# Performance work log

Measured on AMD Instinct MI355X. Metric: run time of the kernel, lower is better.

The kernel has to match this reference:

```python
import jax, jax.numpy as jnp
import numpy as np

EPS = 1e-5

def setup_inputs() -> dict:
    key = jax.random.key(0)
    ks = jax.random.split(key, 6)
    B, S, F, D = 512, 64, 768, 256
    # xavier-ish scales for weights
    return {
        "audio_feat": jax.random.normal(ks[0], (B, S, F), dtype=jnp.float32),
        "visual_feat": jax.random.normal(ks[1], (B, S, F), dtype=jnp.float32),
        "Wa": jax.random.normal(ks[2], (F, D), dtype=jnp.float32) * (1.0 / np.sqrt(F)),
        "ba": jnp.zeros((D,), dtype=jnp.float32),
        "Wv": jax.random.normal(ks[3], (F, D), dtype=jnp.float32) * (1.0 / np.sqrt(F)),
        "bv": jnp.zeros((D,), dtype=jnp.float32),
        "corr": jax.random.normal(ks[4], (D, D), dtype=jnp.float32) * float(np.sqrt(2.0 / (D + D))),
        "Wb": jax.random.normal(ks[5], (2 * D, 64), dtype=jnp.float32) * (1.0 / np.sqrt(2 * D)),
        "bb": jnp.zeros((64,), dtype=jnp.float32),
        "gamma": jnp.ones((64,), dtype=jnp.float32),
        "beta": jnp.zeros((64,), dtype=jnp.float32),
    }


def reference(audio_feat, visual_feat, Wa, ba, Wv, bv, corr, Wb, bb, gamma, beta):
    # project: [b,s,768] -> [b,s,256]
    a = jnp.einsum('bsf,fd->bsd', audio_feat, Wa) + ba      # audio proj
    v = jnp.einsum('bsf,fd->bsd', visual_feat, Wv) + bv     # vision proj
    vT = jnp.swapaxes(v, 1, 2)                              # [b,d,s]
    # bilinear correlation: cc[b,i,j] = a[b,i,:] @ corr @ v[b,j,:]
    cc = jnp.einsum('bid,de,bje->bij', a, corr, v)          # [b,sa,sv]
    audio_att = jax.nn.softmax(cc, axis=1)                  # softmax over audio positions
    visual_att = jax.nn.softmax(cc, axis=2)                 # softmax over visual positions (of cc^T along dim 1)
    # attended features, both [b,d,s]
    att_a = jnp.einsum('bid,bij->bdj', a, audio_att) + jnp.swapaxes(a, 1, 2)
    att_v = jnp.einsum('bdj,bij->bdi', vT, jnp.swapaxes(visual_att, 1, 2))
    # note: bmm(vT [b,d,sv], visual_att^T' ...) -> torch does vT @ visual_att_t where
    # visual_att_t[b,j,i] = visual_att[b,i,j]; equivalent einsum below
    att_v = jnp.einsum('bdj,bji->bdi', vT, jnp.swapaxes(visual_att, 1, 2)) + vT
    fused = jnp.concatenate([att_a, att_v], axis=1)         # [b,2d,s]
    fused = jnp.swapaxes(fused, 1, 2)                       # [b,s,2d]
    h = jnp.einsum('bsk,ko->bso', fused, Wb) + bb           # [b,s,64]
    mu = jnp.mean(h, axis=-1, keepdims=True)
    var = jnp.mean(jnp.square(h - mu), axis=-1, keepdims=True)
    h = (h - mu) * jax.lax.rsqrt(var + EPS) * gamma + beta
    return jax.nn.relu(h)
```

## Files before the change

kernel.cpp:

```cpp
#include <hip/hip_runtime.h>

typedef _Float16 f16x8 __attribute__((ext_vector_type(8)));
typedef _Float16 f16x4 __attribute__((ext_vector_type(4)));
typedef float    f32x4 __attribute__((ext_vector_type(4)));

#define A16_OFF   0u
#define V16_OFF   16777216u
#define WAP_OFF   33554432u
#define WVP_OFF   33947648u
#define CORRT_OFF 34340864u
#define WBT_OFF   34471936u

#define SCHED0() __builtin_amdgcn_sched_barrier(0)
#define SBAR()   __builtin_amdgcn_s_barrier()

__device__ __forceinline__ void gl_lds16(const void* g, void* l) {
    __builtin_amdgcn_global_load_lds(
        (const __attribute__((address_space(1))) void*)g,
        (__attribute__((address_space(3))) void*)l, 16, 0, 0);
}

__global__ __launch_bounds__(256) void k_prep(
    const float* __restrict__ Wa, const float* __restrict__ Wv,
    const float* __restrict__ corr, const float* __restrict__ Wb,
    _Float16* __restrict__ WaP, _Float16* __restrict__ WvP,
    _Float16* __restrict__ corrT, _Float16* __restrict__ WbT)
{
    __shared__ _Float16 tile[64][72];
    int bid = blockIdx.x;
    int t = threadIdx.x;
    if (bid < 192) {
        int z = bid >= 96;
        int b = z ? bid - 96 : bid;
        const float* W = z ? Wv : Wa;
        _Float16* P = z ? WvP : WaP;
        int kc = b >> 2, nbg = b & 3;
        int l = t & 63, sub = t >> 6;
        int nb = nbg * 4 + sub;
        int q = l >> 4, lm = l & 15;
        int k0 = kc * 32 + q * 8;
        int n = nb * 16 + lm;
        _Float16 tmp[8];
        #pragma unroll
        for (int e = 0; e < 8; ++e)
            tmp[e] = (_Float16)W[(size_t)(k0 + e) * 256 + n];
        *reinterpret_cast<f16x8*>(P + ((size_t)(kc * 16 + nb) * 64 + l) * 8) =
            *reinterpret_cast<const f16x8*>(tmp);
    } else {
        int b2 = bid - 192;
        const float* src; _Float16* dst; int R, C, tr, tc;
        if (b2 < 16) { src = corr; dst = corrT; R = 256; C = 256; tr = b2 >> 2; tc = b2 & 3; }
        else         { src = Wb;   dst = WbT;   R = 512; C = 64;  tr = b2 - 16; tc = 0;      }
        int r0 = tr * 64, c0 = tc * 64;
        #pragma unroll
        for (int it = 0; it < 16; ++it) {
            int idx = t + it * 256;
            int r = idx >> 6, c = idx & 63;
            tile[r][c] = (_Float16)src[(size_t)(r0 + r) * C + (c0 + c)];
        }
        __syncthreads();
        #pragma unroll
        for (int it = 0; it < 16; ++it) {
            int idx = t + it * 256;
            int c = idx >> 6, r = idx & 63;
            dst[(size_t)(c0 + c) * R + (r0 + r)] = tile[r][c];
        }
    }
}

__global__ __launch_bounds__(512, 1) void k_proj(
    const float* __restrict__ Xa, const float* __restrict__ Xv,
    const _Float16* __restrict__ WaP, const _Float16* __restrict__ WvP,
    const float* __restrict__ ba, const float* __restrict__ bv,
    _Float16* __restrict__ Aout, _Float16* __restrict__ Vout)
{
    extern __shared__ __align__(16) char smem[];

    const int bid = blockIdx.x;
    const int lin = (bid & 7) * 64 + (bid >> 3);
    const int z = lin >> 8, mb = lin & 255;
    const float*    X    = z ? Xv  : Xa;
    const _Float16* WP   = z ? WvP : WaP;
    const float*    bias = z ? bv  : ba;
    _Float16*       Out  = z ? Vout : Aout;
    const int m0 = mb * 128;

    const int t = threadIdx.x, lane = t & 63, w = t >> 6;
    const int wr = w >> 1, wc = w & 1;
    const int q = lane >> 4, lm = lane & 15;

    f32x4 acc[2][8] = {};

    auto stageA = [&](int ks) {
        char* base = smem + (ks & 3) * 16384;
        #pragma unroll
        for (int it = 0; it < 2; ++it) {
            int idx0 = it * 512 + w * 64;
            int idx = idx0 + lane;
            int r = idx >> 3, c = idx & 7;
            int gc = c ^ (r & 7);
            gl_lds16(X + (size_t)(m0 + r) * 768 + ks * 32 + gc * 4,
                     base + idx0 * 16);
        }
    };
    auto stageB = [&](int ks) {
        char* base = smem + 65536 + (ks & 3) * 16384;
        #pragma unroll
        for (int it = 0; it < 2; ++it) {
            int idx0 = it * 512 + w * 64;
            gl_lds16(WP + ((size_t)ks * 1024 + idx0 + lane) * 8,
                     base + idx0 * 16);
        }
    };

    stageA(0); stageB(0);
    stageA(1); stageB(1);
    stageA(2); stageB(2);
    stageA(3); stageB(3);
    asm volatile("s_waitcnt vmcnt(12)" ::: "memory"); SCHED0();
    SBAR();

    for (int ks = 0; ks < 24; ++ks) {
        const char* Ac = smem + (ks & 3) * 16384;
        const char* Bc = smem + 65536 + (ks & 3) * 16384;

        f16x8 af[2];
        #pragma unroll
        for (int mf = 0; mf < 2; ++mf) {
            int r = wr * 32 + mf * 16 + lm;
            const char* base = Ac + r * 128;
            int c0 = (2 * q) ^ (r & 7);
            int c1 = (2 * q + 1) ^ (r & 7);
            f32x4 lo = *reinterpret_cast<const f32x4*>(base + c0 * 16);
            f32x4 hi = *reinterpret_cast<const f32x4*>(base + c1 * 16);
            f16x4 l4 = __builtin_convertvector(lo, f16x4);
            f16x4 h4 = __builtin_convertvector(hi, f16x4);
            af[mf] = __builtin_shufflevector(l4, h4, 0, 1, 2, 3, 4, 5, 6, 7);
        }
        #pragma unroll
        for (int nf = 0; nf < 8; ++nf) {
            int nb = wc * 8 + nf;
            f16x8 bf = *reinterpret_cast<const f16x8*>(Bc + (nb * 64 + lane) * 16);
            acc[0][nf] = __builtin_amdgcn_mfma_f32_16x16x32_f16(af[0], bf, acc[0][nf], 0, 0, 0);
            acc[1][nf] = __builtin_amdgcn_mfma_f32_16x16x32_f16(af[1], bf, acc[1][nf], 0, 0, 0);
        }
        asm volatile("s_waitcnt lgkmcnt(0)" ::: "memory"); SCHED0();
        SBAR();
        if (ks + 4 < 24) { stageA(ks + 4); stageB(ks + 4); }
        if (ks < 20)      { asm volatile("s_waitcnt vmcnt(12)" ::: "memory"); }
        else if (ks == 20){ asm volatile("s_waitcnt vmcnt(8)"  ::: "memory"); }
        else if (ks == 21){ asm volatile("s_waitcnt vmcnt(4)"  ::: "memory"); }
        else if (ks == 22){ asm volatile("s_waitcnt vmcnt(0)"  ::: "memory"); }
        SCHED0();
        if (ks < 23) SBAR();
    }

    float biasv[8];
    #pragma unroll
    for (int nf = 0; nf < 8; ++nf)
        biasv[nf] = bias[wc * 128 + nf * 16 + lm];

    _Float16* Cs = (_Float16*)smem;
    #pragma unroll
    for (int mf = 0; mf < 2; ++mf)
        #pragma unroll
        for (int nf = 0; nf < 8; ++nf)
            #pragma unroll
            for (int r = 0; r < 4; ++r)
                Cs[(wr * 32 + mf * 16 + q * 4 + r) * 256 + wc * 128 + nf * 16 + lm] =
                    (_Float16)(acc[mf][nf][r] + biasv[nf]);
    __syncthreads();
    #pragma unroll
    for (int it = 0; it < 8; ++it) {
        int idx = t + it * 512;
        int row = idx >> 5, c = idx & 31;
        f16x8 vv = *reinterpret_cast<const f16x8*>(Cs + row * 256 + c * 8);
        *reinterpret_cast<f16x8*>(Out + (size_t)(m0 + row) * 256 + c * 8) = vv;
    }
}

#define SM_A    0u
#define SM_V    33792u
#define SM_AC   67584u
#define SM_CC   101376u
#define SM_ATA  118272u
#define SM_ATV  127488u
#define SM_AWT  136704u
#define SM_VWT  145920u
#define SM_RED  155136u
#define SM_TOTAL 159232u

__global__ __launch_bounds__(256) void k_fuse(
    const _Float16* __restrict__ A16, const _Float16* __restrict__ V16,
    const _Float16* __restrict__ corrT, const _Float16* __restrict__ WbT,
    const float* __restrict__ bb, const float* __restrict__ gamma,
    const float* __restrict__ beta, float* __restrict__ out)
{
    extern __shared__ char sm[];
    _Float16* a_s   = (_Float16*)(sm + SM_A);
    _Float16* v_s   = (_Float16*)(sm + SM_V);
    _Float16* ac_s  = (_Float16*)(sm + SM_AC);
    float*    cc_s  = (float*)(sm + SM_CC);
    _Float16* attAT = (_Float16*)(sm + SM_ATA);
    _Float16* attV  = (_Float16*)(sm + SM_ATV);
    _Float16* awT   = (_Float16*)(sm + SM_AWT);
    _Float16* vwT   = (_Float16*)(sm + SM_VWT);
    float*    red   = (float*)(sm + SM_RED);

    const int b = blockIdx.x;
    const int t = threadIdx.x, lane = t & 63, w = t >> 6;
    const int q = lane >> 4, lm = lane & 15;

    const _Float16* Ab = A16 + (size_t)b * 64 * 256;
    const _Float16* Vb = V16 + (size_t)b * 64 * 256;
    #pragma unroll
    for (int it = 0; it < 8; ++it) {
        int idx = t + it * 256;
        int row = idx >> 5, kc = idx & 31;
        *reinterpret_cast<f16x8*>(a_s + row * 264 + kc * 8) =
            *reinterpret_cast<const f16x8*>(Ab + row * 256 + kc * 8);
        *reinterpret_cast<f16x8*>(v_s + row * 264 + kc * 8) =
            *reinterpret_cast<const f16x8*>(Vb + row * 256 + kc * 8);
    }
    __syncthreads();

    {
        f32x4 acc[4][4] = {};
        for (int ks = 0; ks < 8; ++ks) {
            f16x8 af[4];
            #pragma unroll
            for (int mf = 0; mf < 4; ++mf)
                af[mf] = *reinterpret_cast<const f16x8*>(a_s + (mf * 16 + lm) * 264 + ks * 32 + q * 8);
            #pragma unroll
            for (int nf = 0; nf < 4; ++nf) {
                int e = w * 64 + nf * 16 + lm;
                f16x8 bf = *reinterpret_cast<const f16x8*>(corrT + (size_t)e * 256 + ks * 32 + q * 8);
                #pragma unroll
                for (int mf = 0; mf < 4; ++mf)
                    acc[mf][nf] = __builtin_amdgcn_mfma_f32_16x16x32_f16(af[mf], bf, acc[mf][nf], 0, 0, 0);
            }
        }
        #pragma unroll
        for (int mf = 0; mf < 4; ++mf)
            #pragma unroll
            for (int nf = 0; nf < 4; ++nf)
                #pragma unroll
                for (int r = 0; r < 4; ++r)
                    ac_s[(mf * 16 + 4 * q + r) * 264 + (w * 64 + nf * 16 + lm)] = (_Float16)acc[mf][nf][r];
    }
    __syncthreads();

    {
        f32x4 acc[4] = {};
        for (int ks = 0; ks < 8; ++ks) {
            f16x8 bf = *reinterpret_cast<const f16x8*>(v_s + (w * 16 + lm) * 264 + ks * 32 + q * 8);
            #pragma unroll
            for (int mf = 0; mf < 4; ++mf) {
                f16x8 af = *reinterpret_cast<const f16x8*>(ac_s + (mf * 16 + lm) * 264 + ks * 32 + q * 8);
                acc[mf] = __builtin_amdgcn_mfma_f32_16x16x32_f16(af, bf, acc[mf], 0, 0, 0);
            }
        }
        #pragma unroll
        for (int mf = 0; mf < 4; ++mf)
            #pragma unroll
            for (int r = 0; r < 4; ++r)
                cc_s[(mf * 16 + 4 * q + r) * 66 + (w * 16 + lm)] = acc[mf][r];
    }
    __syncthreads();

    {
        int j = t & 63, seg = w;
        float cmx = -1e30f, rmx = -1e30f;
        #pragma unroll
        for (int k = 0; k < 16; ++k) {
            int i = seg * 16 + k;
            cmx = fmaxf(cmx, cc_s[i * 66 + j]);
            rmx = fmaxf(rmx, cc_s[j * 66 + i]);
        }
        red[0 * 256 + seg * 64 + j] = cmx;
        red[2 * 256 + seg * 64 + j] = rmx;
        __syncthreads();
        float cm = fmaxf(fmaxf(red[0 * 256 + 0 * 64 + j], red[0 * 256 + 1 * 64 + j]),
                         fmaxf(red[0 * 256 + 2 * 64 + j], red[0 * 256 + 3 * 64 + j]));
        float rm = fmaxf(fmaxf(red[2 * 256 + 0 * 64 + j], red[2 * 256 + 1 * 64 + j]),
                         fmaxf(red[2 * 256 + 2 * 64 + j], red[2 * 256 + 3 * 64 + j]));
        float cs = 0.f, rs = 0.f;
        #pragma unroll
        for (int k = 0; k < 16; ++k) {
            int i = seg * 16 + k;
            cs += __expf(cc_s[i * 66 + j] - cm);
            rs += __expf(cc_s[j * 66 + i] - rm);
        }
        red[1 * 256 + seg * 64 + j] = cs;
        red[3 * 256 + seg * 64 + j] = rs;
        __syncthreads();
        float csum = red[1 * 256 + 0 * 64 + j] + red[1 * 256 + 1 * 64 + j] +
                     red[1 * 256 + 2 * 64 + j] + red[1 * 256 + 3 * 64 + j];
        float rsum = red[3 * 256 + 0 * 64 + j] + red[3 * 256 + 1 * 64 + j] +
                     red[3 * 256 + 2 * 64 + j] + red[3 * 256 + 3 * 64 + j];
        float cinv = 1.f / csum, rinv = 1.f / rsum;
        #pragma unroll
        for (int k = 0; k < 16; ++k) {
            int i = seg * 16 + k;
            float pa = __expf(cc_s[i * 66 + j] - cm) * cinv;
            if (i == j) pa += 1.f;
            attAT[j * 72 + i] = (_Float16)pa;
            float pv = __expf(cc_s[j * 66 + i] - rm) * rinv;
            if (i == j) pv += 1.f;
            attV[j * 72 + i] = (_Float16)pv;
        }
    }

    {
        int isV = w >> 1, wcol = w & 1;
        const _Float16* src = isV ? v_s : a_s;
        const int doff = isV ? 256 : 0;
        f32x4 acc[4][2] = {};
        for (int ks = 0; ks < 8; ++ks) {
            f16x8 af[4];
            #pragma unroll
            for (int mf = 0; mf < 4; ++mf)
                af[mf] = *reinterpret_cast<const f16x8*>(src + (mf * 16 + lm) * 264 + ks * 32 + q * 8);
            #pragma unroll
            for (int nf = 0; nf < 2; ++nf) {
                int o = wcol * 32 + nf * 16 + lm;
                f16x8 bf = *reinterpret_cast<const f16x8*>(WbT + (size_t)o * 512 + doff + ks * 32 + q * 8);
                #pragma unroll
                for (int mf = 0; mf < 4; ++mf)
                    acc[mf][nf] = __builtin_amdgcn_mfma_f32_16x16x32_f16(af[mf], bf, acc[mf][nf], 0, 0, 0);
            }
        }
        _Float16* dst = isV ? vwT : awT;
        #pragma unroll
        for (int mf = 0; mf < 4; ++mf)
            #pragma unroll
            for (int nf = 0; nf < 2; ++nf)
                #pragma unroll
                for (int r = 0; r < 4; ++r)
                    dst[(wcol * 32 + nf * 16 + lm) * 72 + (mf * 16 + 4 * q + r)] = (_Float16)acc[mf][nf][r];
    }
    __syncthreads();

    f32x4 hacc[4] = {};
    #pragma unroll
    for (int kk = 0; kk < 2; ++kk) {
        f16x8 a1 = *reinterpret_cast<const f16x8*>(attAT + (16 * w + lm) * 72 + kk * 32 + q * 8);
        f16x8 a2 = *reinterpret_cast<const f16x8*>(attV  + (16 * w + lm) * 72 + kk * 32 + q * 8);
        #pragma unroll
        for (int nf = 0; nf < 4; ++nf) {
            f16x8 b1 = *reinterpret_cast<const f16x8*>(awT + (nf * 16 + lm) * 72 + kk * 32 + q * 8);
            f16x8 b2 = *reinterpret_cast<const f16x8*>(vwT + (nf * 16 + lm) * 72 + kk * 32 + q * 8);
            hacc[nf] = __builtin_amdgcn_mfma_f32_16x16x32_f16(a1, b1, hacc[nf], 0, 0, 0);
            hacc[nf] = __builtin_amdgcn_mfma_f32_16x16x32_f16(a2, b2, hacc[nf], 0, 0, 0);
        }
    }

    {
        float bbv[4], gv[4], bev[4];
        #pragma unroll
        for (int nf = 0; nf < 4; ++nf) {
            int o = nf * 16 + lm;
            bbv[nf] = bb[o]; gv[nf] = gamma[o]; bev[nf] = beta[o];
        }
        #pragma unroll
        for (int r = 0; r < 4; ++r) {
            float vals[4]; float s1 = 0.f, s2 = 0.f;
            #pragma unroll
            for (int nf = 0; nf < 4; ++nf) {
                float hv = hacc[nf][r] + bbv[nf];
                vals[nf] = hv; s1 += hv; s2 += hv * hv;
            }
            #pragma unroll
            for (int m = 1; m < 16; m <<= 1) {
                s1 += __shfl_xor(s1, m, 64);
                s2 += __shfl_xor(s2, m, 64);
            }
            float mu = s1 * 0.015625f;
            float var = s2 * 0.015625f - mu * mu;
            float rstd = rsqrtf(var + 1e-5f);
            int s = 16 * w + 4 * q + r;
            float* orow = out + ((size_t)b * 64 + s) * 64;
            #pragma unroll
            for (int nf = 0; nf < 4; ++nf) {
                float y = (vals[nf] - mu) * rstd * gv[nf] + bev[nf];
                orow[nf * 16 + lm] = fmaxf(y, 0.f);
            }
        }
    }
}

extern "C" void kernel_launch(void* const* d_in, const int* in_sizes, int n_in,
                              void* d_out, int out_size, void* d_ws, size_t ws_size,
                              hipStream_t stream) {
    const float* Xa    = (const float*)d_in[0];
    const float* Xv    = (const float*)d_in[1];
    const float* Wa    = (const float*)d_in[2];
    const float* ba    = (const float*)d_in[3];
    const float* Wv    = (const float*)d_in[4];
    const float* bv    = (const float*)d_in[5];
    const float* corr  = (const float*)d_in[6];
    const float* Wb    = (const float*)d_in[7];
    const float* bb    = (const float*)d_in[8];
    const float* gamma = (const float*)d_in[9];
    const float* beta  = (const float*)d_in[10];
    float* out = (float*)d_out;
    char* ws = (char*)d_ws;

    _Float16* a16   = (_Float16*)(ws + A16_OFF);
    _Float16* v16   = (_Float16*)(ws + V16_OFF);
    _Float16* WaP   = (_Float16*)(ws + WAP_OFF);
    _Float16* WvP   = (_Float16*)(ws + WVP_OFF);
    _Float16* corrT = (_Float16*)(ws + CORRT_OFF);
    _Float16* WbT   = (_Float16*)(ws + WBT_OFF);

    hipLaunchKernelGGL(k_prep, dim3(216), dim3(256), 0, stream,
                       Wa, Wv, corr, Wb, WaP, WvP, corrT, WbT);
    (void)hipFuncSetAttribute((const void*)k_proj,
                              hipFuncAttributeMaxDynamicSharedMemorySize, 131072);
    hipLaunchKernelGGL(k_proj, dim3(512), dim3(512), 131072, stream,
                       Xa, Xv, WaP, WvP, ba, bv, a16, v16);
    (void)hipFuncSetAttribute((const void*)k_fuse,
                              hipFuncAttributeMaxDynamicSharedMemorySize, SM_TOTAL);
    hipLaunchKernelGGL(k_fuse, dim3(512), dim3(256), SM_TOTAL, stream,
                       a16, v16, corrT, WbT, bb, gamma, beta, out);
}
```

Baseline: 92.74 us.

## Restructure projection GEMM pipeline with register-staged A loads and K=64 steps

The projection GEMM's main loop now advances 64 K-elements per step, double-buffered, instead of 32 with a 4-deep LDS ring. The fp32 A tile is loaded into registers three steps ahead and written to swizzled LDS by the threads, rather than copied direct-to-LDS. B still uses direct global-to-LDS loads. The aim is fewer barriers per K and better latency hiding, at the cost of more VGPRs for the staging registers and more complex vmcnt bookkeeping.

New measurement: 99.24 us. +7.0%, slower.

```diff
diff --git a/kernel.cpp b/kernel.cpp
--- a/kernel.cpp
+++ b/kernel.cpp
@@ -13,11 +13,21 @@
 
 #define SCHED0() __builtin_amdgcn_sched_barrier(0)
 #define SBAR()   __builtin_amdgcn_s_barrier()
+#define LGKM0()  do { asm volatile("s_waitcnt lgkmcnt(0)" ::: "memory"); SCHED0(); } while (0)
 
 __device__ __forceinline__ void gl_lds16(const void* g, void* l) {
     __builtin_amdgcn_global_load_lds(
         (const __attribute__((address_space(1))) void*)g,
         (__attribute__((address_space(3))) void*)l, 16, 0, 0);
+}
+
+__device__ __forceinline__ void vwait(int n) {
+    switch (n) {
+        case 0: asm volatile("s_waitcnt vmcnt(0)" ::: "memory"); break;
+        case 4: asm volatile("s_waitcnt vmcnt(4)" ::: "memory"); break;
+        case 8: asm volatile("s_waitcnt vmcnt(8)" ::: "memory"); break;
+        default: asm volatile("s_waitcnt vmcnt(0)" ::: "memory"); break;
+    }
 }
 
 __global__ __launch_bounds__(256) void k_prep(
@@ -89,70 +99,91 @@
     const int wr = w >> 1, wc = w & 1;
     const int q = lane >> 4, lm = lane & 15;
 
+    const float* Xb = X + (size_t)m0 * 768;
+
     f32x4 acc[2][8] = {};
-
-    auto stageA = [&](int ks) {
-        char* base = smem + (ks & 3) * 16384;
-        #pragma unroll
-        for (int it = 0; it < 2; ++it) {
-            int idx0 = it * 512 + w * 64;
-            int idx = idx0 + lane;
-            int r = idx >> 3, c = idx & 7;
-            int gc = c ^ (r & 7);
-            gl_lds16(X + (size_t)(m0 + r) * 768 + ks * 32 + gc * 4,
-                     base + idx0 * 16);
+    f32x4 sA[4], sB[4];
+
+    auto loadA = [&](int ks, f32x4* s) {
+        #pragma unroll
+        for (int j = 0; j < 4; ++j) {
+            int idx = j * 512 + t;
+            int row = idx >> 4, c = idx & 15;
+            s[j] = *reinterpret_cast<const f32x4*>(Xb + (size_t)row * 768 + ks * 64 + c * 4);
         }
     };
-    auto stageB = [&](int ks) {
-        char* base = smem + 65536 + (ks & 3) * 16384;
-        #pragma unroll
-        for (int it = 0; it < 2; ++it) {
-            int idx0 = it * 512 + w * 64;
-            gl_lds16(WP + ((size_t)ks * 1024 + idx0 + lane) * 8,
-                     base + idx0 * 16);
+    auto writeA = [&](int buf, f32x4* s) {
+        #pragma unroll
+        for (int j = 0; j < 4; ++j) {
+            int idx = j * 512 + t;
+            int row = idx >> 4, c = idx & 15;
+            int cs = c ^ ((row & 7) << 1);
+            *reinterpret_cast<f32x4*>(smem + buf * 32768 + row * 256 + cs * 16) = s[j];
         }
     };
-
-    stageA(0); stageB(0);
-    stageA(1); stageB(1);
-    stageA(2); stageB(2);
-    stageA(3); stageB(3);
-    asm volatile("s_waitcnt vmcnt(12)" ::: "memory"); SCHED0();
+    auto stageB = [&](int ks, int buf) {
+        char* base = smem + 65536 + buf * 32768;
+        #pragma unroll
+        for (int it = 0; it < 4; ++it) {
+            int u0 = it * 512 + w * 64;
+            gl_lds16(WP + ((size_t)ks * 2048 + u0 + lane) * 8, base + u0 * 16);
+        }
+    };
+
+    loadA(0, sA); loadA(1, sB);
+    stageB(0, 0); stageB(1, 1);
+    vwait(8); SCHED0();
+    writeA(0, sA); writeA(1, sB);
+    loadA(2, sA);
+    vwait(8); SCHED0();
+    LGKM0();
     SBAR();
 
-    for (int ks = 0; ks < 24; ++ks) {
-        const char* Ac = smem + (ks & 3) * 16384;
-        const char* Bc = smem + 65536 + (ks & 3) * 16384;
-
-        f16x8 af[2];
+    #pragma unroll
+    for (int ks = 0; ks < 12; ++ks) {
+        const int cur = ks & 1;
+        const char* Ac = smem + cur * 32768;
+        const char* Bc = smem + 65536 + cur * 32768;
+
+        f16x8 af[2][2];
         #pragma unroll
         for (int mf = 0; mf < 2; ++mf) {
-            int r = wr * 32 + mf * 16 + lm;
-            const char* base = Ac + r * 128;
-            int c0 = (2 * q) ^ (r & 7);
-            int c1 = (2 * q + 1) ^ (r & 7);
-            f32x4 lo = *reinterpret_cast<const f32x4*>(base + c0 * 16);
-            f32x4 hi = *reinterpret_cast<const f32x4*>(base + c1 * 16);
-            f16x4 l4 = __builtin_convertvector(lo, f16x4);
-            f16x4 h4 = __builtin_convertvector(hi, f16x4);
-            af[mf] = __builtin_shufflevector(l4, h4, 0, 1, 2, 3, 4, 5, 6, 7);
-        }
-        #pragma unroll
-        for (int nf = 0; nf < 8; ++nf) {
-            int nb = wc * 8 + nf;
-            f16x8 bf = *reinterpret_cast<const f16x8*>(Bc + (nb * 64 + lane) * 16);
-            acc[0][nf] = __builtin_amdgcn_mfma_f32_16x16x32_f16(af[0], bf, acc[0][nf], 0, 0, 0);
-            acc[1][nf] = __builtin_amdgcn_mfma_f32_16x16x32_f16(af[1], bf, acc[1][nf], 0, 0, 0);
-        }
-        asm volatile("s_waitcnt lgkmcnt(0)" ::: "memory"); SCHED0();
+            int rr = wr * 32 + mf * 16 + lm;
+            #pragma unroll
+            for (int kk = 0; kk < 2; ++kk) {
+                int c0 = kk * 8 + 2 * q;
+                int cs0 = c0 ^ ((rr & 7) << 1);
+                int cs1 = (c0 + 1) ^ ((rr & 7) << 1);
+                f32x4 lo = *reinterpret_cast<const f32x4*>(Ac + rr * 256 + cs0 * 16);
+                f32x4 hi = *reinterpret_cast<const f32x4*>(Ac + rr * 256 + cs1 * 16);
+                f16x4 l4 = __builtin_convertvector(lo, f16x4);
+                f16x4 h4 = __builtin_convertvector(hi, f16x4);
+                af[mf][kk] = __builtin_shufflevector(l4, h4, 0, 1, 2, 3, 4, 5, 6, 7);
+            }
+        }
+        #pragma unroll
+        for (int kk = 0; kk < 2; ++kk)
+            #pragma unroll
+            for (int nf = 0; nf < 8; ++nf) {
+                int nb = wc * 8 + nf;
+                f16x8 bf = *reinterpret_cast<const f16x8*>(
+                    Bc + (kk * 1024 + nb * 64 + lane) * 16);
+                acc[0][nf] = __builtin_amdgcn_mfma_f32_16x16x32_f16(af[0][kk], bf, acc[0][nf], 0, 0, 0);
+                acc[1][nf] = __builtin_amdgcn_mfma_f32_16x16x32_f16(af[1][kk], bf, acc[1][nf], 0, 0, 0);
+            }
+        LGKM0();
         SBAR();
-        if (ks + 4 < 24) { stageA(ks + 4); stageB(ks + 4); }
-        if (ks < 20)      { asm volatile("s_waitcnt vmcnt(12)" ::: "memory"); }
-        else if (ks == 20){ asm volatile("s_waitcnt vmcnt(8)"  ::: "memory"); }
-        else if (ks == 21){ asm volatile("s_waitcnt vmcnt(4)"  ::: "memory"); }
-        else if (ks == 22){ asm volatile("s_waitcnt vmcnt(0)"  ::: "memory"); }
-        SCHED0();
-        if (ks < 23) SBAR();
+
+        if (ks + 2 < 12) stageB(ks + 2, cur);
+        if (ks + 3 < 12) loadA(ks + 3, (ks & 1) ? sA : sB);
+        if (ks + 2 < 12) {
+            if (ks <= 8) vwait(8); else vwait(4);
+            SCHED0();
+            writeA(cur, (ks & 1) ? sB : sA);
+        } else if (ks == 10) {
+            vwait(0); SCHED0();
+        }
+        if (ks < 11) SBAR();
     }
 
     float biasv[8];
```
